# Kernel tuning notes

Measured on AMD Instinct MI355X. Metric: run time of the kernel, lower is better.

## Reference

```python
import jax, jax.numpy as jnp
import numpy as np

A, C, H, W = 8, 256, 80, 108      # agents, channels, cf_h, cf_w from the module
NUM_CLASSES = 7
OUT_H, OUT_W = 256, 256


def warp_affine(feat, M):
    """Bilinear affine warp of feat [C,H,W] with sampling matrix M [2,3].
    dst(u,v) = src(M @ [u,v,1]); out-of-bounds samples are zero (kornia zero padding)."""
    c, h, w = feat.shape
    vs, us = jnp.meshgrid(jnp.arange(h, dtype=feat.dtype),
                          jnp.arange(w, dtype=feat.dtype), indexing='ij')
    sx = M[0, 0] * us + M[0, 1] * vs + M[0, 2]
    sy = M[1, 0] * us + M[1, 1] * vs + M[1, 2]
    x0 = jnp.floor(sx)
    y0 = jnp.floor(sy)
    wx = sx - x0
    wy = sy - y0
    x0i = x0.astype(jnp.int32)
    y0i = y0.astype(jnp.int32)

    def tap(yy, xx, wgt):
        valid = (yy >= 0) & (yy < h) & (xx >= 0) & (xx < w)
        yyc = jnp.clip(yy, 0, h - 1)
        xxc = jnp.clip(xx, 0, w - 1)
        return feat[:, yyc, xxc] * (wgt * valid)[None]

    return (tap(y0i, x0i, (1 - wy) * (1 - wx))
            + tap(y0i, x0i + 1, (1 - wy) * wx)
            + tap(y0i + 1, x0i, wy * (1 - wx))
            + tap(y0i + 1, x0i + 1, wy * wx))


def resize_bilinear_align_corners(img, oh, ow):
    """F.interpolate(..., mode='bilinear', align_corners=True) for img [N,C,H,W]."""
    h, w = img.shape[-2:]
    ys = jnp.linspace(0.0, h - 1.0, oh, dtype=img.dtype)
    xs = jnp.linspace(0.0, w - 1.0, ow, dtype=img.dtype)
    y0 = jnp.clip(jnp.floor(ys).astype(jnp.int32), 0, h - 2)
    x0 = jnp.clip(jnp.floor(xs).astype(jnp.int32), 0, w - 2)
    wy = (ys - y0)[None, None, :, None]
    wx = (xs - x0)[None, None, None, :]
    row = img[:, :, y0, :] * (1 - wy) + img[:, :, y0 + 1, :] * wy   # [N,C,oh,W]
    return row[:, :, :, x0] * (1 - wx) + row[:, :, :, x0 + 1] * wx  # [N,C,oh,ow]


def setup_inputs() -> dict:
    key = jax.random.key(0)
    k1, k2, k3, k4, k5, k6 = jax.random.split(key, 6)
    x = jax.random.normal(k1, (A, C, H, W), jnp.float32)
    # near-identity per-pair affine sampling matrices with small rotation/shear + translation
    rel = jnp.tile(jnp.eye(2, 3, dtype=jnp.float32), (A, A, 1, 1))
    rel = rel + 0.05 * jax.random.normal(k2, (A, A, 2, 3), jnp.float32)
    rel = rel.at[..., 2].add(10.0 * jax.random.normal(k3, (A, A, 2), jnp.float32))
    adjacency_matrix = jax.random.randint(k4, (A, A), 0, 2, dtype=jnp.int32)
    car_masks = jax.random.uniform(k5, (A, 256, 256), jnp.float32)
    w_cls = 0.02 * jax.random.normal(k6, (NUM_CLASSES, C), jnp.float32)
    b_cls = jnp.zeros((NUM_CLASSES,), jnp.float32)
    return {"x": x, "relative_tfs": rel, "adjacency_matrix": adjacency_matrix,
            "car_masks": car_masks, "w_cls": w_cls, "b_cls": b_cls}


def reference(x, relative_tfs, adjacency_matrix, car_masks, w_cls, b_cls):
    # x = x + F.interpolate(car_masks.unsqueeze(1), (cf_h, cf_w), 'bilinear')  (align_corners=False)
    cm = jax.image.resize(car_masks[:, None], (A, 1, H, W), method="bilinear")
    x = x + cm

    # aggregate_features: per ego-agent i, warp all agents' features into i's frame,
    # zero agents with adjacency[i,j]==0, and sum over j.
    warp_all = jax.vmap(warp_affine)                       # over agents j
    warped = jax.vmap(lambda Ms: warp_all(x, Ms))(relative_tfs)  # [A,A,C,H,W]
    fov = (adjacency_matrix != 0).astype(x.dtype)          # [A,A]
    aggr = jnp.einsum('ij,ijchw->ichw', fov, warped)       # masked sum over j

    def predict(f):  # mask_prediction (1x1 conv) + sigmoid
        logits = jnp.einsum('oc,achw->aohw', w_cls, f) + b_cls[None, :, None, None]
        return jax.nn.sigmoid(logits)

    solo_x = resize_bilinear_align_corners(predict(x), OUT_H, OUT_W)
    aggr_x = resize_bilinear_align_corners(predict(aggr), OUT_H, OUT_W)
    return (solo_x, aggr_x)
```

## Files before the change

kernel.cpp:

```cpp
#include <hip/hip_runtime.h>
#include <hip/hip_bf16.h>

#define A_N 8
#define C_N 256
#define H_N 80
#define W_N 108
#define P_N (H_N * W_N)
#define P4_N (P_N / 4)
#define O_N 7
#define MH 256
#define MW 256
#define OUT_HW 256
#define BPA 135

#define W16OFF(c) ((c) * 8 + ((c) >> 4) * 4)
#define W16SIZE   (C_N * 8 + (C_N / 16) * 4)

__device__ __forceinline__ float sigmoidf_(float zv) {
    return 1.0f / (1.0f + __expf(-zv));
}

__launch_bounds__(256, 2)
__global__ void k_conv(const float* __restrict__ x, const float* __restrict__ masks,
                       const float* __restrict__ w, const float* __restrict__ b,
                       float* __restrict__ z, float* __restrict__ ssolo)
{
    __shared__ float  s_w[W16SIZE];
    __shared__ float4 s_red[4][16][O_N];
    __shared__ float  s_cm[64];

    const int tid  = threadIdx.x;
    const int lane = tid & 63;
    const int wid  = tid >> 6;
    const int a    = blockIdx.x / BPA;
    const int tile = blockIdx.x - a * BPA;

    {
        const int c = tid;
        #pragma unroll
        for (int o = 0; o < 8; ++o)
            s_w[W16OFF(c) + o] = (o < O_N) ? w[o * C_N + c] : 0.0f;
    }

    if (tid < 64) {
        const int p  = tile * 64 + tid;
        const int oy = p / W_N, ox = p - oy * W_N;
        const float ksy = 256.0f / 80.0f;
        const float ksx = 256.0f / 108.0f;
        const float rky = 0.3125f;
        const float rkx = 0.421875f;
        const float sfy = ((float)oy + 0.5f) * ksy - 0.5f;
        const float sfx = ((float)ox + 0.5f) * ksx - 0.5f;
        const int iyS = (int)ceilf(sfy - ksy);
        const int ixS = (int)ceilf(sfx - ksx);

        float wxv[5];
        float wxs = 0.0f;
        #pragma unroll
        for (int q = 0; q < 5; ++q) {
            const int ix = ixS + q;
            float wv = fmaxf(0.0f, 1.0f - fabsf(sfx - (float)ix) * rkx);
            wv = (ix >= 0 && ix < MW) ? wv : 0.0f;
            wxv[q] = wv;
            wxs += wv;
        }
        const float* mp = masks + (size_t)a * (MH * MW);
        float acm = 0.0f, wys = 0.0f;
        #pragma unroll
        for (int r = 0; r < 7; ++r) {
            const int iy = iyS + r;
            float wy = fmaxf(0.0f, 1.0f - fabsf(sfy - (float)iy) * rky);
            wy = (iy >= 0 && iy < MH) ? wy : 0.0f;
            wys += wy;
            const float* row = mp + min(max(iy, 0), MH - 1) * MW;
            float rs = 0.0f;
            #pragma unroll
            for (int q = 0; q < 5; ++q)
                rs = fmaf(wxv[q], row[min(max(ixS + q, 0), MW - 1)], rs);
            acm = fmaf(wy, rs, acm);
        }
        s_cm[tid] = acm / (wys * wxs);
    }
    __syncthreads();

    const int p   = lane & 15;
    const int cs  = lane >> 4;
    const int px4 = tile * 16 + p;
    const int cb  = wid * 64 + cs * 16;

    const float* xp = x + ((size_t)a * C_N + cb) * P_N + (size_t)px4 * 4;

#define LD(k) const float4 v##k = *reinterpret_cast<const float4*>(xp + (size_t)(k) * P_N);
    LD(0)  LD(1)  LD(2)  LD(3)  LD(4)  LD(5)  LD(6)  LD(7)
    LD(8)  LD(9)  LD(10) LD(11) LD(12) LD(13) LD(14) LD(15)
#undef LD

    const float4 cm4 = make_float4(s_cm[p * 4], s_cm[p * 4 + 1],
                                   s_cm[p * 4 + 2], s_cm[p * 4 + 3]);

    float4 acc[O_N];
    #pragma unroll
    for (int o = 0; o < O_N; ++o) acc[o] = make_float4(0.f, 0.f, 0.f, 0.f);

#define FMA(k)                                                                 \
    {                                                                          \
        float4 v = v##k;                                                       \
        v.x += cm4.x; v.y += cm4.y; v.z += cm4.z; v.w += cm4.w;                \
        const float4 wA = *reinterpret_cast<const float4*>(s_w + W16OFF(cb + (k)));     \
        const float4 wB = *reinterpret_cast<const float4*>(s_w + W16OFF(cb + (k)) + 4); \
        acc[0].x = fmaf(wA.x, v.x, acc[0].x); acc[0].y = fmaf(wA.x, v.y, acc[0].y);     \
        acc[0].z = fmaf(wA.x, v.z, acc[0].z); acc[0].w = fmaf(wA.x, v.w, acc[0].w);     \
        acc[1].x = fmaf(wA.y, v.x, acc[1].x); acc[1].y = fmaf(wA.y, v.y, acc[1].y);     \
        acc[1].z = fmaf(wA.y, v.z, acc[1].z); acc[1].w = fmaf(wA.y, v.w, acc[1].w);     \
        acc[2].x = fmaf(wA.z, v.x, acc[2].x); acc[2].y = fmaf(wA.z, v.y, acc[2].y);     \
        acc[2].z = fmaf(wA.z, v.z, acc[2].z); acc[2].w = fmaf(wA.z, v.w, acc[2].w);     \
        acc[3].x = fmaf(wA.w, v.x, acc[3].x); acc[3].y = fmaf(wA.w, v.y, acc[3].y);     \
        acc[3].z = fmaf(wA.w, v.z, acc[3].z); acc[3].w = fmaf(wA.w, v.w, acc[3].w);     \
        acc[4].x = fmaf(wB.x, v.x, acc[4].x); acc[4].y = fmaf(wB.x, v.y, acc[4].y);     \
        acc[4].z = fmaf(wB.x, v.z, acc[4].z); acc[4].w = fmaf(wB.x, v.w, acc[4].w);     \
        acc[5].x = fmaf(wB.y, v.x, acc[5].x); acc[5].y = fmaf(wB.y, v.y, acc[5].y);     \
        acc[5].z = fmaf(wB.y, v.z, acc[5].z); acc[5].w = fmaf(wB.y, v.w, acc[5].w);     \
        acc[6].x = fmaf(wB.z, v.x, acc[6].x); acc[6].y = fmaf(wB.z, v.y, acc[6].y);     \
        acc[6].z = fmaf(wB.z, v.z, acc[6].z); acc[6].w = fmaf(wB.z, v.w, acc[6].w);     \
    }
    FMA(0)  FMA(1)  FMA(2)  FMA(3)  FMA(4)  FMA(5)  FMA(6)  FMA(7)
    FMA(8)  FMA(9)  FMA(10) FMA(11) FMA(12) FMA(13) FMA(14) FMA(15)
#undef FMA

    #pragma unroll
    for (int o = 0; o < O_N; ++o) {
        acc[o].x += __shfl_xor(acc[o].x, 16); acc[o].y += __shfl_xor(acc[o].y, 16);
        acc[o].z += __shfl_xor(acc[o].z, 16); acc[o].w += __shfl_xor(acc[o].w, 16);
        acc[o].x += __shfl_xor(acc[o].x, 32); acc[o].y += __shfl_xor(acc[o].y, 32);
        acc[o].z += __shfl_xor(acc[o].z, 32); acc[o].w += __shfl_xor(acc[o].w, 32);
    }
    if (lane < 16) {
        #pragma unroll
        for (int o = 0; o < O_N; ++o) s_red[wid][lane][o] = acc[o];
    }
    __syncthreads();

    if (tid < 16 * O_N) {
        const int p2 = tid & 15;
        const int o  = tid >> 4;
        const float4 s0 = s_red[0][p2][o];
        const float4 s1 = s_red[1][p2][o];
        const float4 s2 = s_red[2][p2][o];
        const float4 s3 = s_red[3][p2][o];
        float4 zv;
        zv.x = s0.x + s1.x + s2.x + s3.x;
        zv.y = s0.y + s1.y + s2.y + s3.y;
        zv.z = s0.z + s1.z + s2.z + s3.z;
        zv.w = s0.w + s1.w + s2.w + s3.w;
        const float bo = b[o];
        const size_t ob = (size_t)(a * O_N + o) * P4_N + tile * 16 + p2;
        reinterpret_cast<float4*>(z)[ob] = zv;
        float4 sv;
        sv.x = sigmoidf_(zv.x + bo);
        sv.y = sigmoidf_(zv.y + bo);
        sv.z = sigmoidf_(zv.z + bo);
        sv.w = sigmoidf_(zv.w + bo);
        reinterpret_cast<float4*>(ssolo)[ob] = sv;
    }
}

__launch_bounds__(64)
__global__ void k_aggr(const float* __restrict__ z, const float* __restrict__ rel,
                       const int* __restrict__ adj, const float* __restrict__ b,
                       float* __restrict__ saggr)
{
    const int i = blockIdx.x / 135;
    const int p = (blockIdx.x - i * 135) * 64 + threadIdx.x;
    const int vy = p / W_N, ux = p - vy * W_N;
    const float fu = (float)ux, fv = (float)vy;

    float acc[O_N];
    #pragma unroll
    for (int o = 0; o < O_N; ++o) acc[o] = b[o];

    for (int j = 0; j < A_N; ++j) {
        if (adj[i * A_N + j] == 0) continue;
        const float* M = rel + (i * A_N + j) * 6;
        float sx = M[0] * fu + M[1] * fv + M[2];
        float sy = M[3] * fu + M[4] * fv + M[5];
        if (!(sx > -1.0f && sx < (float)W_N && sy > -1.0f && sy < (float)H_N)) continue;
        float x0f = floorf(sx), y0f = floorf(sy);
        float wx = sx - x0f, wy = sy - y0f;
        int x0 = (int)x0f, y0 = (int)y0f;
        int x1 = x0 + 1,  y1 = y0 + 1;
        float w00 = (1.0f - wy) * (1.0f - wx), w01 = (1.0f - wy) * wx;
        float w10 = wy * (1.0f - wx),          w11 = wy * wx;
        if (x0 < 0)    { w00 = 0.0f; w10 = 0.0f; x0 = 0; }
        if (x1 >= W_N) { w01 = 0.0f; w11 = 0.0f; x1 = W_N - 1; }
        if (y0 < 0)    { w00 = 0.0f; w01 = 0.0f; y0 = 0; }
        if (y1 >= H_N) { w10 = 0.0f; w11 = 0.0f; y1 = H_N - 1; }
        const int i00 = y0 * W_N + x0, i01 = y0 * W_N + x1;
        const int i10 = y1 * W_N + x0, i11 = y1 * W_N + x1;
        const float* zj = z + j * O_N * P_N;
        #pragma unroll
        for (int o = 0; o < O_N; ++o) {
            const float* zp = zj + o * P_N;
            acc[o] += w00 * zp[i00] + w01 * zp[i01] + w10 * zp[i10] + w11 * zp[i11];
        }
    }
    const int ob = i * O_N * P_N + p;
    #pragma unroll
    for (int o = 0; o < O_N; ++o) saggr[ob + o * P_N] = sigmoidf_(acc[o]);
}

__launch_bounds__(256)
__global__ void k_upsample(const float* __restrict__ ssolo, const float* __restrict__ saggr,
                           float* __restrict__ out)
{
    const int idx = blockIdx.x * 256 + threadIdx.x;
    int k = idx;
    const int oxq = k & 63;   k >>= 6;
    const int oy  = k & 255;  k >>= 8;
    const int o   = k % O_N;  k /= O_N;
    const int a   = k & 7;    k >>= 3;
    const int t   = k;

    const float* src = (t == 0 ? ssolo : saggr) + (a * O_N + o) * P_N;
    float syf = (float)oy * (79.0f / 255.0f);
    int y0 = (int)syf; y0 = min(y0, H_N - 2);
    float wy = syf - (float)y0;
    const float* r0 = src + y0 * W_N;
    const float* r1 = r0 + W_N;

    float res[4];
    #pragma unroll
    for (int q = 0; q < 4; ++q) {
        int ox = oxq * 4 + q;
        float sxf = (float)ox * (107.0f / 255.0f);
        int x0 = (int)sxf; x0 = min(x0, W_N - 2);
        float wx = sxf - (float)x0;
        float c0 = r0[x0]     * (1.0f - wy) + r1[x0]     * wy;
        float c1 = r0[x0 + 1] * (1.0f - wy) + r1[x0 + 1] * wy;
        res[q] = c0 * (1.0f - wx) + c1 * wx;
    }
    *reinterpret_cast<float4*>(out + (size_t)idx * 4) =
        make_float4(res[0], res[1], res[2], res[3]);
}

extern "C" void kernel_launch(void* const* d_in, const int* in_sizes, int n_in,
                              void* d_out, int out_size, void* d_ws, size_t ws_size,
                              hipStream_t stream)
{
    (void)in_sizes; (void)n_in; (void)out_size; (void)ws_size;
    const float* x    = (const float*)d_in[0];
    const float* rel  = (const float*)d_in[1];
    const int*   adj  = (const int*)d_in[2];
    const float* cmsk = (const float*)d_in[3];
    const float* wcls = (const float*)d_in[4];
    const float* bcls = (const float*)d_in[5];
    float* out = (float*)d_out;

    float* ws    = (float*)d_ws;
    float* z     = ws;
    float* ssolo = z     + A_N * O_N * P_N;
    float* saggr = ssolo + A_N * O_N * P_N;

    k_conv    <<<A_N * BPA, 256, 0, stream>>>(x, cmsk, wcls, bcls, z, ssolo);
    k_aggr    <<<1080, 64, 0, stream>>>(z, rel, adj, bcls, saggr);
    k_upsample<<<7168, 256, 0, stream>>>(ssolo, saggr, out);
}
```

Measured before the change: 39.84 us.

## Split 1x1 conv over channel groups with partial sums and a finalize kernel

Reworks the classifier conv so each block handles 256 pixels and one of four 64-channel groups. Each group writes its partial logits to a workspace, and a new finalize kernel sums the four partials, then writes z and the sigmoid output. The goal is a different load pattern: each lane reads contiguous float4 pixels across channels, which should give wider coalesced reads, and the shuffle reduction is gone. The cost is an extra kernel launch and a write and re-read of a partial-sum buffer four times the size of z. The car-mask resize is now recomputed in each of the four channel-group blocks.

```diff
diff --git a/kernel.cpp b/kernel.cpp
--- a/kernel.cpp
+++ b/kernel.cpp
@@ -11,40 +11,41 @@
 #define MH 256
 #define MW 256
 #define OUT_HW 256
-#define BPA 135
-
-#define W16OFF(c) ((c) * 8 + ((c) >> 4) * 4)
-#define W16SIZE   (C_N * 8 + (C_N / 16) * 4)
+#define TPA 34
+#define NCG 4
 
 __device__ __forceinline__ float sigmoidf_(float zv) {
     return 1.0f / (1.0f + __expf(-zv));
 }
 
 __launch_bounds__(256, 2)
-__global__ void k_conv(const float* __restrict__ x, const float* __restrict__ masks,
-                       const float* __restrict__ w, const float* __restrict__ b,
-                       float* __restrict__ z, float* __restrict__ ssolo)
-{
-    __shared__ float  s_w[W16SIZE];
-    __shared__ float4 s_red[4][16][O_N];
-    __shared__ float  s_cm[64];
+__global__ void k_convp(const float* __restrict__ x, const float* __restrict__ masks,
+                        const float* __restrict__ w, float* __restrict__ part)
+{
+    __shared__ float4 s_red[O_N][NCG][64];
+    __shared__ float  s_w[512];
+    __shared__ float  s_cm[256];
 
     const int tid  = threadIdx.x;
     const int lane = tid & 63;
     const int wid  = tid >> 6;
-    const int a    = blockIdx.x / BPA;
-    const int tile = blockIdx.x - a * BPA;
+    const int bi   = blockIdx.x;
+    const int cg   = bi & 3;
+    const int t2   = bi >> 2;
+    const int tile = t2 % TPA;
+    const int a    = t2 / TPA;
+
+    if (tid < 64) {
+        const int c = cg * 64 + tid;
+        #pragma unroll
+        for (int o = 0; o < 8; ++o)
+            s_w[tid * 8 + o] = (o < O_N) ? w[o * C_N + c] : 0.0f;
+    }
 
     {
-        const int c = tid;
-        #pragma unroll
-        for (int o = 0; o < 8; ++o)
-            s_w[W16OFF(c) + o] = (o < O_N) ? w[o * C_N + c] : 0.0f;
-    }
-
-    if (tid < 64) {
-        const int p  = tile * 64 + tid;
-        const int oy = p / W_N, ox = p - oy * W_N;
+        const int px = tile * 256 + tid;
+        const int pc = min(px, P_N - 1);
+        const int oy = pc / W_N, ox = pc - oy * W_N;
         const float ksy = 256.0f / 80.0f;
         const float ksx = 256.0f / 108.0f;
         const float rky = 0.3125f;
@@ -83,20 +84,16 @@
     }
     __syncthreads();
 
-    const int p   = lane & 15;
-    const int cs  = lane >> 4;
-    const int px4 = tile * 16 + p;
-    const int cb  = wid * 64 + cs * 16;
-
-    const float* xp = x + ((size_t)a * C_N + cb) * P_N + (size_t)px4 * 4;
-
-#define LD(k) const float4 v##k = *reinterpret_cast<const float4*>(xp + (size_t)(k) * P_N);
+    const int px4  = tile * 64 + lane;
+    const int px4c = min(px4, P4_N - 1);
+    const float* xp = x + ((size_t)a * C_N + cg * 64 + wid) * P_N + (size_t)px4c * 4;
+
+#define LD(k) const float4 v##k = *reinterpret_cast<const float4*>(xp + (size_t)(4 * (k)) * P_N);
     LD(0)  LD(1)  LD(2)  LD(3)  LD(4)  LD(5)  LD(6)  LD(7)
     LD(8)  LD(9)  LD(10) LD(11) LD(12) LD(13) LD(14) LD(15)
 #undef LD
 
-    const float4 cm4 = make_float4(s_cm[p * 4], s_cm[p * 4 + 1],
-                                   s_cm[p * 4 + 2], s_cm[p * 4 + 3]);
+    const float4 cm4 = reinterpret_cast<const float4*>(s_cm)[lane];
 
     float4 acc[O_N];
     #pragma unroll
@@ -106,62 +103,76 @@
     {                                                                          \
         float4 v = v##k;                                                       \
         v.x += cm4.x; v.y += cm4.y; v.z += cm4.z; v.w += cm4.w;                \
-        const float4 wA = *reinterpret_cast<const float4*>(s_w + W16OFF(cb + (k)));     \
-        const float4 wB = *reinterpret_cast<const float4*>(s_w + W16OFF(cb + (k)) + 4); \
-        acc[0].x = fmaf(wA.x, v.x, acc[0].x); acc[0].y = fmaf(wA.x, v.y, acc[0].y);     \
-        acc[0].z = fmaf(wA.x, v.z, acc[0].z); acc[0].w = fmaf(wA.x, v.w, acc[0].w);     \
-        acc[1].x = fmaf(wA.y, v.x, acc[1].x); acc[1].y = fmaf(wA.y, v.y, acc[1].y);     \
-        acc[1].z = fmaf(wA.y, v.z, acc[1].z); acc[1].w = fmaf(wA.y, v.w, acc[1].w);     \
-        acc[2].x = fmaf(wA.z, v.x, acc[2].x); acc[2].y = fmaf(wA.z, v.y, acc[2].y);     \
-        acc[2].z = fmaf(wA.z, v.z, acc[2].z); acc[2].w = fmaf(wA.z, v.w, acc[2].w);     \
-        acc[3].x = fmaf(wA.w, v.x, acc[3].x); acc[3].y = fmaf(wA.w, v.y, acc[3].y);     \
-        acc[3].z = fmaf(wA.w, v.z, acc[3].z); acc[3].w = fmaf(wA.w, v.w, acc[3].w);     \
-        acc[4].x = fmaf(wB.x, v.x, acc[4].x); acc[4].y = fmaf(wB.x, v.y, acc[4].y);     \
-        acc[4].z = fmaf(wB.x, v.z, acc[4].z); acc[4].w = fmaf(wB.x, v.w, acc[4].w);     \
-        acc[5].x = fmaf(wB.y, v.x, acc[5].x); acc[5].y = fmaf(wB.y, v.y, acc[5].y);     \
-        acc[5].z = fmaf(wB.y, v.z, acc[5].z); acc[5].w = fmaf(wB.y, v.w, acc[5].w);     \
-        acc[6].x = fmaf(wB.z, v.x, acc[6].x); acc[6].y = fmaf(wB.z, v.y, acc[6].y);     \
-        acc[6].z = fmaf(wB.z, v.z, acc[6].z); acc[6].w = fmaf(wB.z, v.w, acc[6].w);     \
+        const float* wc = s_w + (wid + 4 * (k)) * 8;         \
+        const float4 wA = *reinterpret_cast<const float4*>(wc);                \
+        const float4 wB = *reinterpret_cast<const float4*>(wc + 4);            \
+        acc[0].x = fmaf(wA.x, v.x, acc[0].x); acc[0].y = fmaf(wA.x, v.y, acc[0].y); \
+        acc[0].z = fmaf(wA.x, v.z, acc[0].z); acc[0].w = fmaf(wA.x, v.w, acc[0].w); \
+        acc[1].x = fmaf(wA.y, v.x, acc[1].x); acc[1].y = fmaf(wA.y, v.y, acc[1].y); \
+        acc[1].z = fmaf(wA.y, v.z, acc[1].z); acc[1].w = fmaf(wA.y, v.w, acc[1].w); \
+        acc[2].x = fmaf(wA.z, v.x, acc[2].x); acc[2].y = fmaf(wA.z, v.y, acc[2].y); \
+        acc[2].z = fmaf(wA.z, v.z, acc[2].z); acc[2].w = fmaf(wA.z, v.w, acc[2].w); \
+        acc[3].x = fmaf(wA.w, v.x, acc[3].x); acc[3].y = fmaf(wA.w, v.y, acc[3].y); \
+        acc[3].z = fmaf(wA.w, v.z, acc[3].z); acc[3].w = fmaf(wA.w, v.w, acc[3].w); \
+        acc[4].x = fmaf(wB.x, v.x, acc[4].x); acc[4].y = fmaf(wB.x, v.y, acc[4].y); \
+        acc[4].z = fmaf(wB.x, v.z, acc[4].z); acc[4].w = fmaf(wB.x, v.w, acc[4].w); \
+        acc[5].x = fmaf(wB.y, v.x, acc[5].x); acc[5].y = fmaf(wB.y, v.y, acc[5].y); \
+        acc[5].z = fmaf(wB.y, v.z, acc[5].z); acc[5].w = fmaf(wB.y, v.w, acc[5].w); \
+        acc[6].x = fmaf(wB.z, v.x, acc[6].x); acc[6].y = fmaf(wB.z, v.y, acc[6].y); \
+        acc[6].z = fmaf(wB.z, v.z, acc[6].z); acc[6].w = fmaf(wB.z, v.w, acc[6].w); \
     }
     FMA(0)  FMA(1)  FMA(2)  FMA(3)  FMA(4)  FMA(5)  FMA(6)  FMA(7)
     FMA(8)  FMA(9)  FMA(10) FMA(11) FMA(12) FMA(13) FMA(14) FMA(15)
 #undef FMA
 
     #pragma unroll
-    for (int o = 0; o < O_N; ++o) {
-        acc[o].x += __shfl_xor(acc[o].x, 16); acc[o].y += __shfl_xor(acc[o].y, 16);
-        acc[o].z += __shfl_xor(acc[o].z, 16); acc[o].w += __shfl_xor(acc[o].w, 16);
-        acc[o].x += __shfl_xor(acc[o].x, 32); acc[o].y += __shfl_xor(acc[o].y, 32);
-        acc[o].z += __shfl_xor(acc[o].z, 32); acc[o].w += __shfl_xor(acc[o].w, 32);
-    }
-    if (lane < 16) {
-        #pragma unroll
-        for (int o = 0; o < O_N; ++o) s_red[wid][lane][o] = acc[o];
-    }
+    for (int o = 0; o < O_N; ++o)
+        s_red[o][wid][lane] = acc[o];
     __syncthreads();
 
-    if (tid < 16 * O_N) {
-        const int p2 = tid & 15;
-        const int o  = tid >> 4;
-        const float4 s0 = s_red[0][p2][o];
-        const float4 s1 = s_red[1][p2][o];
-        const float4 s2 = s_red[2][p2][o];
-        const float4 s3 = s_red[3][p2][o];
-        float4 zv;
-        zv.x = s0.x + s1.x + s2.x + s3.x;
-        zv.y = s0.y + s1.y + s2.y + s3.y;
-        zv.z = s0.z + s1.z + s2.z + s3.z;
-        zv.w = s0.w + s1.w + s2.w + s3.w;
-        const float bo = b[o];
-        const size_t ob = (size_t)(a * O_N + o) * P4_N + tile * 16 + p2;
-        reinterpret_cast<float4*>(z)[ob] = zv;
-        float4 sv;
-        sv.x = sigmoidf_(zv.x + bo);
-        sv.y = sigmoidf_(zv.y + bo);
-        sv.z = sigmoidf_(zv.z + bo);
-        sv.w = sigmoidf_(zv.w + bo);
-        reinterpret_cast<float4*>(ssolo)[ob] = sv;
-    }
+    for (int pair = tid; pair < 64 * O_N; pair += 256) {
+        const int pl = pair & 63;
+        const int o  = pair >> 6;
+        const int pg = tile * 64 + pl;
+        if (pg >= P4_N) continue;
+        const float4 s0 = s_red[o][0][pl];
+        const float4 s1 = s_red[o][1][pl];
+        const float4 s2 = s_red[o][2][pl];
+        const float4 s3 = s_red[o][3][pl];
+        float4 pv;
+        pv.x = s0.x + s1.x + s2.x + s3.x;
+        pv.y = s0.y + s1.y + s2.y + s3.y;
+        pv.z = s0.z + s1.z + s2.z + s3.z;
+        pv.w = s0.w + s1.w + s2.w + s3.w;
+        reinterpret_cast<float4*>(part)[((size_t)(cg * A_N + a) * O_N + o) * P4_N + pg] = pv;
+    }
+}
+
+__launch_bounds__(256)
+__global__ void k_finalize(const float* __restrict__ part, const float* __restrict__ b,
+                           float* __restrict__ z, float* __restrict__ ssolo)
+{
+    const int id = blockIdx.x * 256 + threadIdx.x;
+    if (id >= A_N * O_N * P4_N) return;
+    const int px4 = id % P4_N;
+    const int ao  = id / P4_N;
+    const int o   = ao % O_N;
+
+    const float4* p4 = reinterpret_cast<const float4*>(part);
+    float4 s = p4[((size_t)(0 * A_N * O_N) + ao) * P4_N + px4];
+    #pragma unroll
+    for (int g = 1; g < NCG; ++g) {
+        const float4 t = p4[((size_t)(g * A_N * O_N) + ao) * P4_N + px4];
+        s.x += t.x; s.y += t.y; s.z += t.z; s.w += t.w;
+    }
+    reinterpret_cast<float4*>(z)[(size_t)ao * P4_N + px4] = s;
+    const float bo = b[o];
+    float4 sv;
+    sv.x = sigmoidf_(s.x + bo);
+    sv.y = sigmoidf_(s.y + bo);
+    sv.z = sigmoidf_(s.z + bo);
+    sv.w = sigmoidf_(s.w + bo);
+    reinterpret_cast<float4*>(ssolo)[(size_t)ao * P4_N + px4] = sv;
 }
 
 __launch_bounds__(64)
@@ -256,11 +267,13 @@
     float* out = (float*)d_out;
 
     float* ws    = (float*)d_ws;
-    float* z     = ws;
+    float* part  = ws;
+    float* z     = part  + NCG * A_N * O_N * P_N;
     float* ssolo = z     + A_N * O_N * P_N;
     float* saggr = ssolo + A_N * O_N * P_N;
 
-    k_conv    <<<A_N * BPA, 256, 0, stream>>>(x, cmsk, wcls, bcls, z, ssolo);
+    k_convp   <<<A_N * TPA * NCG, 256, 0, stream>>>(x, cmsk, wcls, part);
+    k_finalize<<<(A_N * O_N * P4_N + 255) / 256, 256, 0, stream>>>(part, bcls, z, ssolo);
     k_aggr    <<<1080, 64, 0, stream>>>(z, rel, adj, bcls, saggr);
     k_upsample<<<7168, 256, 0, stream>>>(ssolo, saggr, out);
 }
```

Result: slower. 43.36 us (+8.9%).
